# Optimization experiments

Measured on AMD Instinct MI355X. Metric: run time of the kernel, lower is better.

## Reference

```python
import jax, jax.numpy as jnp
import numpy as np

N = 100_000      # nodes
E = 1_600_000    # edges
F_IN = 4         # num_features
H = 128          # hidden_channels
C = 5            # num_classes
G = 256          # graphs in batch


def setup_inputs() -> dict:
    key = jax.random.key(0)
    ks = jax.random.split(key, 14)
    x = jax.random.normal(ks[0], (N, F_IN), dtype=jnp.float32)
    edge_index = jax.random.randint(ks[1], (2, E), 0, N, dtype=jnp.int64)
    batch = jnp.sort(jax.random.randint(ks[2], (N,), 0, G, dtype=jnp.int64))
    def lin(k, fan_in, fan_out):
        kw, kb = jax.random.split(k)
        s = 1.0 / np.sqrt(fan_in)
        W = jax.random.uniform(kw, (fan_in, fan_out), jnp.float32, -s, s)
        b = jax.random.uniform(kb, (fan_out,), jnp.float32, -s, s)
        return W, b
    W1, b1 = lin(ks[3], F_IN, H)
    W2, b2 = lin(ks[4], H, H)
    W3, b3 = lin(ks[5], H, H)
    W4, b4 = lin(ks[6], H, H)
    Wl, bl = lin(ks[7], H, C)
    return {"x": x, "edge_index": edge_index, "batch": batch,
            "W1": W1, "b1": b1, "W2": W2, "b2": b2,
            "W3": W3, "b3": b3, "W4": W4, "b4": b4,
            "Wl": Wl, "bl": bl}


def reference(x, edge_index, batch, W1, b1, W2, b2, W3, b3, W4, b4, Wl, bl):
    n = x.shape[0]
    loop = jnp.arange(n, dtype=edge_index.dtype)
    src = jnp.concatenate([edge_index[0], loop])  # [E+N], with self-loops
    dst = jnp.concatenate([edge_index[1], loop])
    # symmetric normalization on A + I (PyG GCNConv default)
    deg = jax.ops.segment_sum(jnp.ones_like(dst, dtype=x.dtype), dst, num_segments=n)
    dinv = deg ** -0.5  # deg >= 1 thanks to self-loops
    coef = dinv[src] * dinv[dst]  # per-edge norm [E+N]

    def conv(h, W, b):
        h = h @ W                               # [N, H]
        msg = h[src] * coef[:, None]            # gather + scale [E+N, H]
        return jax.ops.segment_sum(msg, dst, num_segments=n) + b

    h = jax.nn.relu(conv(x, W1, b1))
    h = jax.nn.relu(conv(h, W2, b2))
    h = jax.nn.relu(conv(h, W3, b3))
    h = jax.nn.relu(conv(h, W4, b4))

    # global_mean_pool over graph ids
    counts = jax.ops.segment_sum(jnp.ones((n,), h.dtype), batch, num_segments=G)
    pooled = jax.ops.segment_sum(h, batch, num_segments=G)
    pooled = pooled / jnp.maximum(counts, 1.0)[:, None]  # [G, H]

    return jax.nn.sigmoid(pooled @ Wl + bl)  # [G, C]
```

## Files before the change

kernel.cpp:

```cpp
#include <hip/hip_runtime.h>
#include <hip/hip_fp8.h>
#include <math.h>

#define N_NODES 100000
#define N_EDGES 1600000
#define F_IN    4
#define HID     128
#define N_CLS   5
#define N_GRAPH 256
#define POOL_SEG 8

#define BSHIFT   9
#define BSIZE    512
#define NBUK     196
#define NCHUNK   200
#define CHUNK    8000

typedef _Float16 f16;
typedef _Float16 f16x2 __attribute__((ext_vector_type(2)));
typedef _Float16 f16x8 __attribute__((ext_vector_type(8)));
typedef float f32x4 __attribute__((ext_vector_type(4)));

__device__ __forceinline__ float rec_coef(unsigned r) {
    return (float)__builtin_bit_cast(_Float16, (unsigned short)(r & 0x7FFFu));
}

__device__ __forceinline__ f16x2 rec_coef2(unsigned r) {
    unsigned c = r & 0x7FFFu;
    return __builtin_bit_cast(f16x2, (c << 16) | c);
}

__device__ __forceinline__ float2 fp8x2_to_f32x2(unsigned short raw) {
    __hip_fp8x2_e4m3 t;
    t.__x = raw;
    return static_cast<float2>(t);
}

#if __has_builtin(__builtin_amdgcn_cvt_pk_f16_fp8)
__device__ __forceinline__ f16x2 cvt_h2(unsigned v) {
    auto t = __builtin_amdgcn_cvt_pk_f16_fp8((short)v);
    return __builtin_bit_cast(f16x2, t);
}
#else
__device__ __forceinline__ f16x2 cvt_h2(unsigned v) {
    float2 f = fp8x2_to_f32x2((unsigned short)v);
    auto t = __builtin_amdgcn_cvt_pkrtz(f.x, f.y);
    return __builtin_bit_cast(f16x2, t);
}
#endif

__device__ __forceinline__ void fma8h(f16x2 c2, uint2 v, f16x2* acc) {
    acc[0] += c2 * cvt_h2(v.x);
    acc[1] += c2 * cvt_h2(v.x >> 16);
    acc[2] += c2 * cvt_h2(v.y);
    acc[3] += c2 * cvt_h2(v.y >> 16);
}

__device__ __forceinline__ f16x2 shfl_xor_h2(f16x2 a, int m) {
    return __builtin_bit_cast(f16x2, __shfl_xor(__builtin_bit_cast(int, a), m, 64));
}

__global__ __launch_bounds__(256) void k_bc(const int* __restrict__ dst, int* __restrict__ C) {
    __shared__ int cnt[NBUK];
    int t = threadIdx.x;
    if (t < NBUK) cnt[t] = 0;
    __syncthreads();
    int base = blockIdx.x * CHUNK;
#pragma unroll
    for (int it = 0; it < 32; ++it) {
        int idx = it * 256 + t;
        if (idx < CHUNK) atomicAdd(&cnt[dst[base + idx] >> BSHIFT], 1);
    }
    __syncthreads();
    if (t < NBUK) C[blockIdx.x * NBUK + t] = cnt[t];
}

__global__ __launch_bounds__(256) void k_bscan(const int* __restrict__ C, int* __restrict__ Off,
                                               int* __restrict__ bbase) {
    __shared__ int s[256];
    int b = threadIdx.x;
    int tot = 0;
    if (b < NBUK) {
        for (int c = 0; c < NCHUNK; ++c) {
            Off[c * NBUK + b] = tot;
            tot += C[c * NBUK + b];
        }
    }
    s[b] = (b < NBUK) ? tot : 0;
    __syncthreads();
    for (int off = 1; off < 256; off <<= 1) {
        int v = (b >= off) ? s[b - off] : 0;
        __syncthreads();
        s[b] += v;
        __syncthreads();
    }
    if (b < NBUK) bbase[b] = s[b] - tot;
    if (b == 0) bbase[NBUK] = N_EDGES;
}

__global__ __launch_bounds__(256) void k_scatter(const int* __restrict__ src, const int* __restrict__ dst,
                                                 const int* __restrict__ Off, const int* __restrict__ bbase,
                                                 unsigned* __restrict__ bkt) {
    __shared__ int cur[NBUK];
    int t = threadIdx.x;
    if (t < NBUK) cur[t] = bbase[t] + Off[blockIdx.x * NBUK + t];
    __syncthreads();
    int base = blockIdx.x * CHUNK;
#pragma unroll
    for (int it = 0; it < 32; ++it) {
        int idx = it * 256 + t;
        if (idx < CHUNK) {
            int s = src[base + idx], d = dst[base + idx];
            int b = d >> BSHIFT;
            int p = atomicAdd(&cur[b], 1);
            bkt[p] = ((unsigned)s << BSHIFT) | (unsigned)(d & (BSIZE - 1));
        }
    }
}

__global__ __launch_bounds__(256) void k_hist2(const unsigned* __restrict__ bkt,
                                               const int* __restrict__ bbase,
                                               int* __restrict__ deg, float* __restrict__ dinv,
                                               int* __restrict__ padTot) {
    __shared__ int hist[BSIZE];
    __shared__ int tot;
    int t = threadIdx.x, b = blockIdx.x;
    hist[t] = 0; hist[t + 256] = 0;
    if (t == 0) tot = 0;
    __syncthreads();
    int s0 = bbase[b], s1 = bbase[b + 1];
    for (int e = s0 + t; e < s1; e += 256) atomicAdd(&hist[bkt[e] & (BSIZE - 1)], 1);
    __syncthreads();
    int loc = 0;
#pragma unroll
    for (int h = 0; h < 2; ++h) {
        int l = t + h * 256;
        int node = b * BSIZE + l;
        int d = hist[l];
        if (node < N_NODES) {
            deg[node] = d;
            dinv[node] = rsqrtf((float)d + 1.0f);
        }
        loc += (d + 15) >> 4;
    }
    atomicAdd(&tot, loc);
    __syncthreads();
    if (t == 0) padTot[b] = tot << 4;
}

__global__ __launch_bounds__(256) void k_pscan(const int* __restrict__ padTot, int* __restrict__ padBase,
                                               int* __restrict__ rowptrP) {
    __shared__ int s[256];
    int b = threadIdx.x;
    int v = (b < NBUK) ? padTot[b] : 0;
    s[b] = v;
    __syncthreads();
    for (int off = 1; off < 256; off <<= 1) {
        int u = (b >= off) ? s[b - off] : 0;
        __syncthreads();
        s[b] += u;
        __syncthreads();
    }
    if (b < NBUK) padBase[b] = s[b] - v;
    if (b == 0) {
        padBase[NBUK] = s[NBUK - 1];
        rowptrP[N_NODES] = s[NBUK - 1];
    }
}

__global__ __launch_bounds__(256) void k_local2(const unsigned* __restrict__ bkt,
                                                const int* __restrict__ bbase,
                                                const int* __restrict__ deg,
                                                const float* __restrict__ dinv,
                                                const int* __restrict__ padBase,
                                                int* __restrict__ rowptrP,
                                                unsigned* __restrict__ edges) {
    __shared__ int sc[BSIZE];
    __shared__ int cur[BSIZE];
    __shared__ int st[BSIZE];
    __shared__ float dv[BSIZE];
    int t = threadIdx.x, b = blockIdx.x;
    int base = padBase[b];
    int n0 = b * BSIZE + t, n1 = n0 + 256;
    int d0 = (n0 < N_NODES) ? deg[n0] : 0;
    int d1 = (n1 < N_NODES) ? deg[n1] : 0;
    int p0 = ((d0 + 15) >> 4) << 4;
    int p1 = ((d1 + 15) >> 4) << 4;
    sc[t] = p0; sc[t + 256] = p1;
    dv[t] = (n0 < N_NODES) ? dinv[n0] : 0.f;
    dv[t + 256] = (n1 < N_NODES) ? dinv[n1] : 0.f;
    __syncthreads();
    for (int off = 1; off < BSIZE; off <<= 1) {
        int i0 = t, i1 = t + 256;
        int v0 = (i0 >= off) ? sc[i0 - off] : 0;
        int v1 = (i1 >= off) ? sc[i1 - off] : 0;
        __syncthreads();
        sc[i0] += v0; sc[i1] += v1;
        __syncthreads();
    }
    int off0 = base + sc[t] - p0;
    int off1 = base + sc[t + 256] - p1;
    if (n0 < N_NODES) rowptrP[n0] = off0;
    if (n1 < N_NODES) rowptrP[n1] = off1;
    cur[t] = off0; cur[t + 256] = off1;
    st[t]  = off0; st[t + 256]  = off1;
    int padT = sc[BSIZE - 1];
    for (int i = base + t; i < base + padT; i += 256) edges[i] = 0;
    __syncthreads();
    int s0 = bbase[b], s1 = bbase[b + 1];
    for (int e = s0 + t; e < s1; e += 256) {
        unsigned r = bkt[e];
        int dl = (int)(r & (BSIZE - 1));
        int s = (int)(r >> BSHIFT);
        int p = atomicAdd(&cur[dl], 1);
        int rs = st[dl];
        int sl = p - rs;
        int phys = rs + (sl & ~15) + (((sl & 3) << 2) | ((sl >> 2) & 3));
        float c = dv[dl] * dinv[s];
        unsigned short cb = __builtin_bit_cast(unsigned short, (f16)c);
        edges[phys] = ((unsigned)s << 15) | (unsigned)(cb & 0x7FFFu);
    }
}

__global__ __launch_bounds__(256) void k_aggx1(const float4* __restrict__ x,
                                               const int* __restrict__ rowptrP,
                                               const unsigned* __restrict__ edges,
                                               const float* __restrict__ dinv,
                                               const float* __restrict__ W1, const float* __restrict__ b1,
                                               unsigned* __restrict__ hA) {
    __shared__ float4 sxa[16];
    __shared__ float sW[4 * HID];
    __shared__ float sb[HID];
    int t = threadIdx.x;
    sW[t] = W1[t];
    sW[t + 256] = W1[t + 256];
    if (t < HID) sb[t] = b1[t];
    int grp = t >> 4;
    int l = t & 15;
    int node = blockIdx.x * 16 + grp;
    int beg = rowptrP[node], end = rowptrP[node + 1];
    float ax = 0.f, ay = 0.f, az = 0.f, aw = 0.f;
    for (int e = beg + l; e < end; e += 16) {
        unsigned r = edges[e];
        float c = rec_coef(r);
        float4 v = x[r >> 15];
        ax = fmaf(c, v.x, ax); ay = fmaf(c, v.y, ay);
        az = fmaf(c, v.z, az); aw = fmaf(c, v.w, aw);
    }
#pragma unroll
    for (int off = 1; off < 16; off <<= 1) {
        ax += __shfl_xor(ax, off, 64);
        ay += __shfl_xor(ay, off, 64);
        az += __shfl_xor(az, off, 64);
        aw += __shfl_xor(aw, off, 64);
    }
    if (l == 0) {
        float di = dinv[node];
        float c0 = di * di;
        float4 xv = x[node];
        sxa[grp] = make_float4(fmaf(c0, xv.x, ax), fmaf(c0, xv.y, ay),
                               fmaf(c0, xv.z, az), fmaf(c0, xv.w, aw));
    }
    __syncthreads();

    int node0 = blockIdx.x * 16;
#pragma unroll
    for (int it = 0; it < 2; ++it) {
        int id = it * 256 + t;
        int n = id >> 5;
        int g = id & 31;
        float4 a = sxa[n];
        float c[4];
#pragma unroll
        for (int j = 0; j < 4; ++j) {
            int col = g * 4 + j;
            float v = sb[col];
            v = fmaf(a.x, sW[col],           v);
            v = fmaf(a.y, sW[HID + col],     v);
            v = fmaf(a.z, sW[2 * HID + col], v);
            v = fmaf(a.w, sW[3 * HID + col], v);
            c[j] = fmaxf(v, 0.0f);
        }
        unsigned lo = __hip_fp8x2_e4m3(make_float2(c[0], c[1])).__x;
        unsigned hi = __hip_fp8x2_e4m3(make_float2(c[2], c[3])).__x;
        hA[(node0 + n) * 32 + g] = lo | (hi << 16);
    }
}

template <bool FP8OUT>
__global__ __launch_bounds__(1024, 8) void k_aggemm8(const unsigned* __restrict__ h8,
                                                     const int* __restrict__ rowptrP,
                                                     const unsigned* __restrict__ edges,
                                                     const float* __restrict__ dinv,
                                                     const f16* __restrict__ Wp,
                                                     const float* __restrict__ bias,
                                                     void* __restrict__ outv) {
    __shared__ f16 S[16 * HID];
    int wave = threadIdx.x >> 6;
    int lane = threadIdx.x & 63;
    int node0 = blockIdx.x * 16;
    int node = node0 + wave;
    int g = lane >> 4;
    int l = lane & 15;
    int beg = __builtin_amdgcn_readfirstlane(rowptrP[node]);
    int end = __builtin_amdgcn_readfirstlane(rowptrP[node + 1]);
    const char* hp = (const char*)h8 + l * 8;

    f16x2 acc[4];
    acc[0] = (f16x2){0, 0}; acc[1] = (f16x2){0, 0};
    acc[2] = (f16x2){0, 0}; acc[3] = (f16x2){0, 0};
    {
        float di = dinv[node];
        f16 c0 = (g == 0) ? (f16)(di * di) : (f16)0.f;
        f16x2 c02; c02.x = c0; c02.y = c0;
        uint2 v = *(const uint2*)(hp + ((size_t)node << 7));
        fma8h(c02, v, acc);
    }

    for (int e = beg; e < end; e += 16) {
        uint4 R = *(const uint4*)(edges + e + g * 4);
        unsigned rr[4] = {R.x, R.y, R.z, R.w};
#pragma unroll
        for (int i = 0; i < 4; ++i) {
            unsigned rec = rr[i];
            uint2 v = *(const uint2*)(hp + ((rec >> 8) & 0xFFFFFF80u));
            fma8h(rec_coef2(rec), v, acc);
        }
    }

#pragma unroll
    for (int j = 0; j < 4; ++j) {
        acc[j] += shfl_xor_h2(acc[j], 16);
        acc[j] += shfl_xor_h2(acc[j], 32);
    }
    if (lane < 16) {
        f16x8 o;
        o[0] = acc[0][0]; o[1] = acc[0][1]; o[2] = acc[1][0]; o[3] = acc[1][1];
        o[4] = acc[2][0]; o[5] = acc[2][1]; o[6] = acc[3][0]; o[7] = acc[3][1];
        int dw = (l * 4) ^ ((wave & 7) << 2);
        *(f16x8*)&S[wave * HID + dw * 2] = o;
    }
    __syncthreads();

    if (wave < 8) {
        int t = wave;
        int m = lane & 15;
        int q = lane >> 4;
        f32x4 c4 = (f32x4){0.f, 0.f, 0.f, 0.f};
#pragma unroll
        for (int ks = 0; ks < 4; ++ks) {
            int dw = (ks * 16 + q * 4) ^ ((m & 7) << 2);
            f16x8 a = *(const f16x8*)&S[m * HID + dw * 2];
            f16x8 b = *(const f16x8*)(Wp + ((size_t)(t * 4 + ks) * 64 + lane) * 8);
            c4 = __builtin_amdgcn_mfma_f32_16x16x32_f16(a, b, c4, 0, 0, 0);
        }
        float bb = bias[t * 16 + m];
#pragma unroll
        for (int r = 0; r < 4; ++r) {
            float val = fmaxf(c4[r] + bb, 0.0f);
            int row = node0 + q * 4 + r;
            if constexpr (FP8OUT) {
                ((__hip_fp8_e4m3*)outv)[(size_t)row * HID + t * 16 + m] = __hip_fp8_e4m3(val);
            } else {
                ((f16*)outv)[(size_t)row * HID + t * 16 + m] = (f16)val;
            }
        }
    }
}

__global__ __launch_bounds__(256) void k_packW3(const float* __restrict__ W2, const float* __restrict__ W3,
                                                const float* __restrict__ W4, f16* __restrict__ Wp) {
    int idx = blockIdx.x * 256 + threadIdx.x;
    int which = idx >> 14;
    int r = idx & 16383;
    const float* W = (which == 0) ? W2 : (which == 1) ? W3 : W4;
    int j  = r & 7;
    int L  = (r >> 3) & 63;
    int ks = (r >> 9) & 3;
    int ct = r >> 11;
    int k = ks * 32 + (L >> 4) * 8 + j;
    int n = ct * 16 + (L & 15);
    Wp[idx] = (f16)W[k * HID + n];
}

__device__ __forceinline__ int lower_bound_batch(const int* __restrict__ batch, int val) {
    int lo = 0, hi = N_NODES;
    while (lo < hi) { int m = (lo + hi) >> 1; if (batch[m] < val) lo = m + 1; else hi = m; }
    return lo;
}

__global__ __launch_bounds__(128) void k_pool1(const f16* __restrict__ h, const int* __restrict__ batch,
                                               float* __restrict__ partials) {
    int g = blockIdx.x / POOL_SEG;
    int s = blockIdx.x % POOL_SEG;
    int f = threadIdx.x;
    int beg = lower_bound_batch(batch, g);
    int end = lower_bound_batch(batch, g + 1);
    int len = end - beg;
    int sb = beg + (int)(((long long)len * s) / POOL_SEG);
    int se = beg + (int)(((long long)len * (s + 1)) / POOL_SEG);
    float acc = 0.0f;
    for (int i = sb; i < se; ++i) acc += (float)h[i * HID + f];
    partials[(size_t)blockIdx.x * HID + f] = acc;
}

__global__ __launch_bounds__(128) void k_pool2h(const float* __restrict__ partials,
                                                const int* __restrict__ batch,
                                                const float* __restrict__ Wl, const float* __restrict__ bl,
                                                float* __restrict__ out) {
    __shared__ float sp[HID];
    int g = blockIdx.x;
    int f = threadIdx.x;
    float acc = 0.0f;
#pragma unroll
    for (int s = 0; s < POOL_SEG; ++s)
        acc += partials[(size_t)(g * POOL_SEG + s) * HID + f];
    int beg = lower_bound_batch(batch, g);
    int end = lower_bound_batch(batch, g + 1);
    sp[f] = acc / fmaxf((float)(end - beg), 1.0f);
    __syncthreads();
    if (f < N_CLS) {
        float v = bl[f];
        for (int k = 0; k < HID; ++k) v = fmaf(sp[k], Wl[k * N_CLS + f], v);
        out[g * N_CLS + f] = 1.0f / (1.0f + expf(-v));
    }
}

extern "C" void kernel_launch(void* const* d_in, const int* in_sizes, int n_in,
                              void* d_out, int out_size, void* d_ws, size_t ws_size,
                              hipStream_t stream) {
    const float* x     = (const float*)d_in[0];
    const int*   ei    = (const int*)d_in[1];
    const int*   batch = (const int*)d_in[2];
    const float* W1 = (const float*)d_in[3];  const float* b1 = (const float*)d_in[4];
    const float* W2 = (const float*)d_in[5];  const float* b2 = (const float*)d_in[6];
    const float* W3 = (const float*)d_in[7];  const float* b3 = (const float*)d_in[8];
    const float* W4 = (const float*)d_in[9];  const float* b4 = (const float*)d_in[10];
    const float* Wl = (const float*)d_in[11]; const float* bl = (const float*)d_in[12];
    float* out = (float*)d_out;

    const size_t EPAD = (size_t)N_EDGES + (size_t)N_NODES * 16;

    char* p = (char*)d_ws;
    auto alloc = [&](size_t bytes) { char* r = p; p += (bytes + 255) & ~(size_t)255; return (void*)r; };
    int*      C       = (int*)     alloc((size_t)NCHUNK * NBUK * 4);
    int*      Off     = (int*)     alloc((size_t)NCHUNK * NBUK * 4);
    int*      bbase   = (int*)     alloc((size_t)(NBUK + 1) * 4);
    int*      padTot  = (int*)     alloc((size_t)NBUK * 4);
    int*      padBase = (int*)     alloc((size_t)(NBUK + 1) * 4);
    unsigned* bkt     = (unsigned*)alloc((size_t)N_EDGES * 4);
    int*      deg     = (int*)     alloc((size_t)N_NODES * 4);
    int*      rowptrP = (int*)     alloc((size_t)(N_NODES + 1) * 4);
    float*    dinv    = (float*)   alloc((size_t)N_NODES * 4);
    unsigned* edges   = (unsigned*)alloc(EPAD * 4);
    unsigned* hA      = (unsigned*)alloc((size_t)N_NODES * HID);
    unsigned* hC      = (unsigned*)alloc((size_t)N_NODES * HID);
    f16*      h4      = (f16*)     alloc((size_t)N_NODES * HID * 2);
    float*    parts   = (float*)   alloc((size_t)N_GRAPH * POOL_SEG * HID * 4);
    f16*      Wp      = (f16*)     alloc((size_t)3 * HID * HID * 2);
    f16*      Wp2 = Wp;
    f16*      Wp3 = Wp + HID * HID;
    f16*      Wp4 = Wp + 2 * HID * HID;

    const int* srcv = ei;
    const int* dstv = ei + N_EDGES;

    k_bc     <<<NCHUNK, 256, 0, stream>>>(dstv, C);
    k_bscan  <<<1, 256, 0, stream>>>(C, Off, bbase);
    k_scatter<<<NCHUNK, 256, 0, stream>>>(srcv, dstv, Off, bbase, bkt);
    k_hist2  <<<NBUK, 256, 0, stream>>>(bkt, bbase, deg, dinv, padTot);
    k_pscan  <<<1, 256, 0, stream>>>(padTot, padBase, rowptrP);
    k_local2 <<<NBUK, 256, 0, stream>>>(bkt, bbase, deg, dinv, padBase, rowptrP, edges);

    k_packW3<<<192, 256, 0, stream>>>(W2, W3, W4, Wp);

    k_aggx1<<<N_NODES / 16, 256, 0, stream>>>((const float4*)x, rowptrP, edges, dinv, W1, b1, hA);

    const int fgrid = N_NODES / 16;
    k_aggemm8<true ><<<fgrid, 1024, 0, stream>>>(hA, rowptrP, edges, dinv, Wp2, b2, hC);
    k_aggemm8<true ><<<fgrid, 1024, 0, stream>>>(hC, rowptrP, edges, dinv, Wp3, b3, hA);
    k_aggemm8<false><<<fgrid, 1024, 0, stream>>>(hA, rowptrP, edges, dinv, Wp4, b4, h4);

    k_pool1 <<<N_GRAPH * POOL_SEG, 128, 0, stream>>>(h4, batch, parts);
    k_pool2h<<<N_GRAPH, 128, 0, stream>>>(parts, batch, Wl, bl, out);
}
```

Before: 360.4 us.

## Process two nodes per wave in fused aggregate-GEMM kernel

Each 64-lane wave now aggregates two destination nodes, one per half-wave, taking 8 edges per iteration instead of 16. Each block covers 32 nodes, so all 16 waves take part in the MFMA projection stage rather than only 8. The shuffle reduction drops to a single xor step. In exchange, the edge-loop bounds are no longer wave-uniform: the two halves can diverge, and the wave runs for the larger of the two node degrees.

```diff
diff --git a/kernel.cpp b/kernel.cpp
--- a/kernel.cpp
+++ b/kernel.cpp
@@ -295,15 +295,17 @@
                                                      const f16* __restrict__ Wp,
                                                      const float* __restrict__ bias,
                                                      void* __restrict__ outv) {
-    __shared__ f16 S[16 * HID];
+    __shared__ f16 S[32 * HID];
     int wave = threadIdx.x >> 6;
     int lane = threadIdx.x & 63;
-    int node0 = blockIdx.x * 16;
-    int node = node0 + wave;
-    int g = lane >> 4;
-    int l = lane & 15;
-    int beg = __builtin_amdgcn_readfirstlane(rowptrP[node]);
-    int end = __builtin_amdgcn_readfirstlane(rowptrP[node + 1]);
+    int half = lane >> 5;
+    int g    = (lane >> 4) & 1;
+    int l    = lane & 15;
+    int node0 = blockIdx.x * 32;
+    int row   = wave * 2 + half;
+    int node  = node0 + row;
+    int beg = rowptrP[node];
+    int end = rowptrP[node + 1];
     const char* hp = (const char*)h8 + l * 8;
 
     f16x2 acc[4];
@@ -317,7 +319,7 @@
         fma8h(c02, v, acc);
     }
 
-    for (int e = beg; e < end; e += 16) {
+    for (int e = beg; e < end; e += 8) {
         uint4 R = *(const uint4*)(edges + e + g * 4);
         unsigned rr[4] = {R.x, R.y, R.z, R.w};
 #pragma unroll
@@ -329,28 +331,27 @@
     }
 
 #pragma unroll
-    for (int j = 0; j < 4; ++j) {
-        acc[j] += shfl_xor_h2(acc[j], 16);
-        acc[j] += shfl_xor_h2(acc[j], 32);
-    }
-    if (lane < 16) {
+    for (int j = 0; j < 4; ++j) acc[j] += shfl_xor_h2(acc[j], 16);
+
+    if ((lane & 16) == 0) {
         f16x8 o;
         o[0] = acc[0][0]; o[1] = acc[0][1]; o[2] = acc[1][0]; o[3] = acc[1][1];
         o[4] = acc[2][0]; o[5] = acc[2][1]; o[6] = acc[3][0]; o[7] = acc[3][1];
-        int dw = (l * 4) ^ ((wave & 7) << 2);
-        *(f16x8*)&S[wave * HID + dw * 2] = o;
-    }
-    __syncthreads();
-
-    if (wave < 8) {
-        int t = wave;
+        int dw = (l * 4) ^ ((row & 7) << 2);
+        *(f16x8*)&S[row * HID + dw * 2] = o;
+    }
+    __syncthreads();
+
+    {
+        int t  = wave >> 1;
+        int rt = wave & 1;
         int m = lane & 15;
         int q = lane >> 4;
         f32x4 c4 = (f32x4){0.f, 0.f, 0.f, 0.f};
 #pragma unroll
         for (int ks = 0; ks < 4; ++ks) {
             int dw = (ks * 16 + q * 4) ^ ((m & 7) << 2);
-            f16x8 a = *(const f16x8*)&S[m * HID + dw * 2];
+            f16x8 a = *(const f16x8*)&S[(rt * 16 + m) * HID + dw * 2];
             f16x8 b = *(const f16x8*)(Wp + ((size_t)(t * 4 + ks) * 64 + lane) * 8);
             c4 = __builtin_amdgcn_mfma_f32_16x16x32_f16(a, b, c4, 0, 0, 0);
         }
@@ -358,11 +359,11 @@
 #pragma unroll
         for (int r = 0; r < 4; ++r) {
             float val = fmaxf(c4[r] + bb, 0.0f);
-            int row = node0 + q * 4 + r;
+            int orow = node0 + rt * 16 + q * 4 + r;
             if constexpr (FP8OUT) {
-                ((__hip_fp8_e4m3*)outv)[(size_t)row * HID + t * 16 + m] = __hip_fp8_e4m3(val);
+                ((__hip_fp8_e4m3*)outv)[(size_t)orow * HID + t * 16 + m] = __hip_fp8_e4m3(val);
             } else {
-                ((f16*)outv)[(size_t)row * HID + t * 16 + m] = (f16)val;
+                ((f16*)outv)[(size_t)orow * HID + t * 16 + m] = (f16)val;
             }
         }
     }
@@ -476,7 +477,7 @@
 
     k_aggx1<<<N_NODES / 16, 256, 0, stream>>>((const float4*)x, rowptrP, edges, dinv, W1, b1, hA);
 
-    const int fgrid = N_NODES / 16;
+    const int fgrid = N_NODES / 32;
     k_aggemm8<true ><<<fgrid, 1024, 0, stream>>>(hA, rowptrP, edges, dinv, Wp2, b2, hC);
     k_aggemm8<true ><<<fgrid, 1024, 0, stream>>>(hC, rowptrP, edges, dinv, Wp3, b3, hA);
     k_aggemm8<false><<<fgrid, 1024, 0, stream>>>(hA, rowptrP, edges, dinv, Wp4, b4, h4);
```

Result: faster. 347.0 us (-3.7%).
